# Kernel tuning notes

Measured on AMD Instinct MI355X. Metric: run time of the kernel, lower is better.

Reference implementation:

```python
import jax, jax.numpy as jnp
import numpy as np


def conv1d(x, w, b):
    # x: (N, Cin, W), w: (Cout, Cin, K) -> (N, Cout, W-K+1), VALID conv (torch Conv1d)
    y = jax.lax.conv_general_dilated(x, w, (1,), 'VALID', dimension_numbers=('NCH', 'OIH', 'NCH'))
    return y + b[None, :, None]


def cnn_block(x, w, b):
    # conv1d then MaxPool1d over the full valid length -> (N, Cout)
    return jnp.max(conv1d(x, w, b), axis=2)


def highway(x, Wp, bp, Wg, bg):
    p = jax.nn.relu(x @ Wp.T + bp)
    g = jax.nn.sigmoid(x @ Wg.T + bg)
    return g * p + (1.0 - g) * x


def lstm_masked(x, lens, Wih, Whh, bih, bhh):
    # x: (N, Wt, E); lens: (N,) valid lengths. Emulates pack_padded_sequence +
    # nn.LSTM + pad_packed_sequence: outputs are h_t for t < len, zeros after.
    N, Wt, _ = x.shape
    H = Whh.shape[1]
    bias = bih + bhh
    h0 = jnp.zeros((N, H), x.dtype)

    def step(carry, inp):
        xt, t = inp
        h, c = carry
        z = xt @ Wih.T + h @ Whh.T + bias  # (N, 4H), gate order i,f,g,o
        i, f, g, o = jnp.split(z, 4, axis=-1)
        c2 = jax.nn.sigmoid(f) * c + jax.nn.sigmoid(i) * jnp.tanh(g)
        h2 = jax.nn.sigmoid(o) * jnp.tanh(c2)
        valid = (t < lens)[:, None]
        h2 = jnp.where(valid, h2, h)
        c2 = jnp.where(valid, c2, c)
        return (h2, c2), jnp.where(valid, h2, jnp.zeros_like(h2))

    xs = jnp.moveaxis(x, 1, 0)  # (Wt, N, E)
    ts = jnp.arange(Wt)
    _, out = jax.lax.scan(step, (h0, h0), (xs, ts))
    return jnp.moveaxis(out, 0, 1)  # (N, Wt, H)


def setup_inputs() -> dict:
    key = jax.random.key(0)
    ks = jax.random.split(key, 32)
    B, T = 32, 48
    WL, WA, WE = 33, 50, 30
    EL, EA, EE, H = 300, 988, 20, 128
    CL, CA, CE = 128, 256, 64
    s = 0.02
    inp = {
        'x_lin': jax.random.normal(ks[0], (B, T, WL, EL), jnp.float32),
        'x_aco': jax.random.normal(ks[1], (B, T, WA, EA), jnp.float32),
        'x_emo': jax.random.normal(ks[2], (B, T, WE, EE), jnp.float32),
        'window_length': jax.random.randint(ks[3], (B, T), 0, WE).astype(jnp.int32) + 1,
        'length': jax.random.randint(ks[4], (B,), 1, T + 1).astype(jnp.int32),
        # CNN params
        'convL_w': s * jax.random.normal(ks[5], (CL, EL, 5), jnp.float32),
        'convL_b': jnp.zeros((CL,), jnp.float32),
        'convA_w': s * jax.random.normal(ks[6], (CA, EA, 10), jnp.float32),
        'convA_b': jnp.zeros((CA,), jnp.float32),
        'convE_w': s * jax.random.normal(ks[7], (CE, H, 3), jnp.float32),
        'convE_b': jnp.zeros((CE,), jnp.float32),
        # Highway params
        'hwL_Wp': s * jax.random.normal(ks[8], (CL, CL), jnp.float32),
        'hwL_bp': jnp.zeros((CL,), jnp.float32),
        'hwL_Wg': s * jax.random.normal(ks[9], (CL, CL), jnp.float32),
        'hwL_bg': jnp.zeros((CL,), jnp.float32),
        'hwA_Wp': s * jax.random.normal(ks[10], (CA, CA), jnp.float32),
        'hwA_bp': jnp.zeros((CA,), jnp.float32),
        'hwA_Wg': s * jax.random.normal(ks[11], (CA, CA), jnp.float32),
        'hwA_bg': jnp.zeros((CA,), jnp.float32),
        'hwE_Wp': s * jax.random.normal(ks[12], (CE, CE), jnp.float32),
        'hwE_bp': jnp.zeros((CE,), jnp.float32),
        'hwE_Wg': s * jax.random.normal(ks[13], (CE, CE), jnp.float32),
        'hwE_bg': jnp.zeros((CE,), jnp.float32),
        # LSTM params (nn.LSTM, 1 layer, batch_first)
        'lstm_Wih': s * jax.random.normal(ks[14], (4 * H, EE), jnp.float32),
        'lstm_Whh': s * jax.random.normal(ks[15], (4 * H, H), jnp.float32),
        'lstm_bih': jnp.zeros((4 * H,), jnp.float32),
        'lstm_bhh': jnp.zeros((4 * H,), jnp.float32),
    }
    return inp


def reference(x_lin, x_aco, x_emo, window_length, length,
              convL_w, convL_b, convA_w, convA_b, convE_w, convE_b,
              hwL_Wp, hwL_bp, hwL_Wg, hwL_bg,
              hwA_Wp, hwA_bp, hwA_Wg, hwA_bg,
              hwE_Wp, hwE_bp, hwE_Wg, hwE_bg,
              lstm_Wih, lstm_Whh, lstm_bih, lstm_bhh):
    B, T = x_lin.shape[:2]
    # Linguistic: per-window CNN + Highway (dropout = identity in eval)
    xl = x_lin.reshape(B * T, x_lin.shape[2], x_lin.shape[3]).transpose(0, 2, 1)  # (BT, 300, WL)
    outL = highway(cnn_block(xl, convL_w, convL_b), hwL_Wp, hwL_bp, hwL_Wg, hwL_bg)
    outL = outL.reshape(B, T, -1)
    # Acoustic
    xa = x_aco.reshape(B * T, x_aco.shape[2], x_aco.shape[3]).transpose(0, 2, 1)  # (BT, 988, WA)
    outA = highway(cnn_block(xa, convA_w, convA_b), hwA_Wp, hwA_bp, hwA_Wg, hwA_bg)
    outA = outA.reshape(B, T, -1)
    # Emotient: ragged per-window LSTM (packed semantics) -> CNN -> Highway
    xe = x_emo.reshape(B * T, x_emo.shape[2], x_emo.shape[3])  # (BT, WE, 20)
    lens = window_length.reshape(B * T)
    h = lstm_masked(xe, lens, lstm_Wih, lstm_Whh, lstm_bih, lstm_bhh)  # (BT, WE, 128)
    outE = highway(cnn_block(h.transpose(0, 2, 1), convE_w, convE_b), hwE_Wp, hwE_bp, hwE_Wg, hwE_bg)
    outE = outE.reshape(B, T, -1)
    # Concatenate modalities -> (B, T, 128+256+64) fed to the downstream head
    return jnp.concatenate([outL, outA, outE], axis=2)
```

## Files before the change

kernel.cpp:

```cpp
#include <hip/hip_runtime.h>
#include <hip/hip_bf16.h>
#include <math.h>

#define BTOT 1536
#define EL 300
#define ELP 320
#define WL_ 33
#define CL 128
#define LOUTL 29
#define KPL 1600
#define EA 988
#define EAP 992
#define WA_ 50
#define CA 256
#define LOUTA 41
#define KPA 9920
#define EE 20
#define WE_ 30
#define HH 128
#define CE 64
#define LOUTE 28
#define KPE 384
#define KDIML 1500
#define KDIMA 9880
#define KDIME 384

typedef __attribute__((ext_vector_type(4))) float f32x4;
typedef __attribute__((ext_vector_type(8))) short short8;

__device__ __forceinline__ unsigned short f2bf(float f) {
    unsigned int x = __float_as_uint(f);
    unsigned int r = (x + 0x7fffu + ((x >> 16) & 1u)) >> 16;
    return (unsigned short)r;
}

__device__ __forceinline__ float sigmf(float x) {
    return __builtin_amdgcn_rcpf(1.f + __expf(-x));
}
__device__ __forceinline__ float tanh_fast(float x) {
    return 1.f - 2.f * __builtin_amdgcn_rcpf(1.f + __expf(2.f * x));
}

#define GLD16(gp, lp) __builtin_amdgcn_global_load_lds( \
    (const __attribute__((address_space(1))) void*)(gp), \
    (__attribute__((address_space(3))) void*)(lp), 16, 0, 0)

template<int N> __device__ __forceinline__ void vmwait() {
    if constexpr (N == 0) asm volatile("s_waitcnt vmcnt(0)" ::: "memory");
    else if constexpr (N == 1) asm volatile("s_waitcnt vmcnt(1)" ::: "memory");
    else if constexpr (N == 2) asm volatile("s_waitcnt vmcnt(2)" ::: "memory");
    else if constexpr (N == 4) asm volatile("s_waitcnt vmcnt(4)" ::: "memory");
    else if constexpr (N == 5) asm volatile("s_waitcnt vmcnt(5)" ::: "memory");
    else if constexpr (N == 6) asm volatile("s_waitcnt vmcnt(6)" ::: "memory");
    else if constexpr (N == 8) asm volatile("s_waitcnt vmcnt(8)" ::: "memory");
    else static_assert(N == 0, "add case");
}

__device__ __forceinline__ void tr_one(const float* a, float* at, int R, int C, int idx) {
    int r = idx / C, c = idx - r * C;
    at[c * R + r] = a[idx];
}
template<int CIN, int CINP, int KW, int COUT, int KPAD>
__device__ __forceinline__ void wt_one(const float* w, unsigned short* wt, int idx) {
    int co = idx / KPAD;
    int p  = idx - co * KPAD;
    int k  = p / CINP;
    int c  = p - k * CINP;
    float v = 0.f;
    if (k < KW && c < CIN) v = w[(co * CIN + c) * KW + k];
    wt[idx] = f2bf(v);
}
template<bool BIG>
__global__ void prep_all(const float* hwL_Wp, float* WpTL, const float* hwL_Wg, float* WgTL,
                         const float* hwA_Wp, float* WpTA, const float* hwA_Wg, float* WgTA,
                         const float* hwE_Wp, float* WpTE, const float* hwE_Wg, float* WgTE,
                         const float* lstm_Wih, float* WihT, const float* lstm_Whh, float* WhhT,
                         const float* convL_w, unsigned short* wtL,
                         const float* convE_w, unsigned short* wtE,
                         const float* convA_w, unsigned short* wtA,
                         unsigned short* whh_bf, unsigned short* wihp_bf) {
    constexpr int S1 = 16384, S2 = 16384, S3 = 65536, S4 = 65536, S5 = 4096, S6 = 4096;
    constexpr int S7 = 512 * 20, S8 = 512 * 128;
    constexpr int S9 = 128 * KPL, S10 = 64 * KPE, S11 = 512 * 128, S12 = 512 * 32;
    constexpr int S13 = CA * KPA;
    constexpr int SMALL = S1 + S2 + S3 + S4 + S5 + S6 + S7 + S8;
    constexpr int TOTAL = BIG ? (SMALL + S9 + S10 + S11 + S12 + S13) : SMALL;
    int stride = gridDim.x * blockDim.x;
    for (int i = blockIdx.x * blockDim.x + threadIdx.x; i < TOTAL; i += stride) {
        int idx = i;
        if (idx < S1) { tr_one(hwL_Wp, WpTL, 128, 128, idx); continue; } idx -= S1;
        if (idx < S2) { tr_one(hwL_Wg, WgTL, 128, 128, idx); continue; } idx -= S2;
        if (idx < S3) { tr_one(hwA_Wp, WpTA, 256, 256, idx); continue; } idx -= S3;
        if (idx < S4) { tr_one(hwA_Wg, WgTA, 256, 256, idx); continue; } idx -= S4;
        if (idx < S5) { tr_one(hwE_Wp, WpTE, 64, 64, idx); continue; } idx -= S5;
        if (idx < S6) { tr_one(hwE_Wg, WgTE, 64, 64, idx); continue; } idx -= S6;
        if (idx < S7) { tr_one(lstm_Wih, WihT, 512, 20, idx); continue; } idx -= S7;
        if (idx < S8) { tr_one(lstm_Whh, WhhT, 512, 128, idx); continue; } idx -= S8;
        if constexpr (BIG) {
            if (idx < S9) { wt_one<EL, ELP, 5, CL, KPL>(convL_w, wtL, idx); continue; } idx -= S9;
            if (idx < S10) { wt_one<HH, HH, 3, CE, KPE>(convE_w, wtE, idx); continue; } idx -= S10;
            if (idx < S11) { whh_bf[idx] = f2bf(lstm_Whh[idx]); continue; } idx -= S11;
            if (idx < S12) { int col = idx >> 5, e = idx & 31;
                             wihp_bf[idx] = (e < 20) ? f2bf(lstm_Wih[col * 20 + e]) : (unsigned short)0;
                             continue; } idx -= S12;
            wt_one<EA, EAP, 10, CA, KPA>(convA_w, wtA, idx);
        }
    }
}

template<int CIN, int CINP>
__device__ __forceinline__ void cvt_chunk(const float* in, unsigned short* out, int idx) {
    constexpr int CH = CINP / 8;
    int row = idx / CH, c0 = (idx - row * CH) * 8;
    const float* src = in + (size_t)row * CIN + c0;
    union { short8 s; unsigned short u[8]; } o;
    if (c0 + 8 <= CIN) {
        float4 v0 = *(const float4*)src;
        float4 v1 = *(const float4*)(src + 4);
        o.u[0]=f2bf(v0.x); o.u[1]=f2bf(v0.y); o.u[2]=f2bf(v0.z); o.u[3]=f2bf(v0.w);
        o.u[4]=f2bf(v1.x); o.u[5]=f2bf(v1.y); o.u[6]=f2bf(v1.z); o.u[7]=f2bf(v1.w);
    } else {
        #pragma unroll
        for (int j = 0; j < 8; ++j) o.u[j] = (c0 + j < CIN) ? f2bf(src[j]) : (unsigned short)0;
    }
    *(short8*)(out + (size_t)row * CINP + c0) = o.s;
}

#define LSTM_BLOCKS 96
#define CVT_BLOCKS 1952

__global__ __launch_bounds__(512, 1)
void lstm_cvt(const float* __restrict__ x_emo,
              const unsigned short* __restrict__ wihp_bf, const unsigned short* __restrict__ whh_bf,
              const float* __restrict__ bih, const float* __restrict__ bhh,
              const int* __restrict__ lens, unsigned short* __restrict__ hbuf,
              const float* __restrict__ xa, const float* __restrict__ xl,
              unsigned short* __restrict__ outa, unsigned short* __restrict__ outl)
{
    __shared__ __align__(16) unsigned short xq[WE_ * 16 * 32];
    __shared__ __align__(16) char h_s[2 * 16 * HH * 2];

    if (blockIdx.x >= LSTM_BLOCKS) {
        constexpr int NAC = (BTOT * WA_) * (EAP / 8);
        constexpr int NLC = (BTOT * WL_) * (ELP / 8);
        int stride = CVT_BLOCKS * 512;
        for (int i = (blockIdx.x - LSTM_BLOCKS) * 512 + threadIdx.x; i < NAC + NLC; i += stride) {
            if (i < NAC) cvt_chunk<EA, EAP>(xa, outa, i);
            else         cvt_chunk<EL, ELP>(xl, outl, i - NAC);
        }
        return;
    }

    const int tid  = threadIdx.x;
    const int w    = tid >> 6;
    const int lane = tid & 63;
    const int lr   = lane & 15;
    const int lq   = lane >> 4;
    const int s0   = blockIdx.x * 16;
    const int c    = w * 16 + lr;

    short8 bfr[4][4];
    short8 bw[4];
    float bj[4];
    #pragma unroll
    for (int g = 0; g < 4; ++g) {
        int col = g * 128 + c;
        #pragma unroll
        for (int kt = 0; kt < 4; ++kt)
            bfr[g][kt] = *(const short8*)(whh_bf + (size_t)col * 128 + kt * 32 + lq * 8);
        bw[g] = *(const short8*)(wihp_bf + (size_t)col * 32 + lq * 8);
        bj[g] = bih[col] + bhh[col];
    }
    int len4[4];
    #pragma unroll
    for (int j = 0; j < 4; ++j) len4[j] = lens[s0 + lq * 4 + j];

    for (int i = tid; i < WE_ * 16 * 32; i += 512) {
        int t = i >> 9, r = (i >> 5) & 15, e = i & 31;
        xq[i] = (e < 20) ? f2bf(x_emo[(((size_t)(s0 + r) * WE_) + t) * 20 + e]) : (unsigned short)0;
    }
    for (int i = tid; i < 2048; i += 512) ((unsigned int*)h_s)[i] = 0u;

    float c_prev[4] = {0.f, 0.f, 0.f, 0.f};
    unsigned short hb_prev[4] = {0, 0, 0, 0};
    __syncthreads();

    for (int t = 0; t < WE_; ++t) {
        const char* hsr = h_s + (t & 1) * 4096;
        char* hsw = h_s + ((t & 1) ^ 1) * 4096;
        short8 ax = *(const short8*)((const char*)xq + (size_t)(t * 16 + lr) * 64 + lq * 16);
        short8 af[4];
        #pragma unroll
        for (int kt = 0; kt < 4; ++kt)
            af[kt] = *(const short8*)(hsr + ((lr * 256 + kt * 64 + lq * 16) ^ ((lr & 7) << 4)));
        f32x4 acc[4];
        #pragma unroll
        for (int g = 0; g < 4; ++g)
            acc[g] = __builtin_amdgcn_mfma_f32_16x16x32_bf16(ax, bw[g], (f32x4){0.f,0.f,0.f,0.f}, 0, 0, 0);
        #pragma unroll
        for (int kt = 0; kt < 4; ++kt)
            #pragma unroll
            for (int g = 0; g < 4; ++g)
                acc[g] = __builtin_amdgcn_mfma_f32_16x16x32_bf16(af[kt], bfr[g][kt], acc[g], 0, 0, 0);
        #pragma unroll
        for (int j = 0; j < 4; ++j) {
            int s = lq * 4 + j;
            float zi = acc[0][j] + bj[0];
            float zf = acc[1][j] + bj[1];
            float zg = acc[2][j] + bj[2];
            float zo = acc[3][j] + bj[3];
            float si = sigmf(zi), sf = sigmf(zf), so = sigmf(zo);
            float tg = tanh_fast(zg);
            float c2 = sf * c_prev[j] + si * tg;
            float h2 = so * tanh_fast(c2);
            bool valid = (t < len4[j]);
            c_prev[j] = valid ? c2 : c_prev[j];
            unsigned short h2b = f2bf(h2);
            unsigned short hn = valid ? h2b : hb_prev[j];
            hb_prev[j] = hn;
            *(unsigned short*)(hsw + (((s * HH + c) * 2) ^ ((s & 7) << 4))) = hn;
            hbuf[(((size_t)(s0 + s) * WE_) + t) * HH + c] = valid ? h2b : (unsigned short)0;
        }
        __syncthreads();
    }
}

template<int LOUT, int WIN, int CINP, int KW, int BN, int NS, int MFR, int COUT>
__global__ __launch_bounds__(256, 2)
void conv_pool_v8(const unsigned short* __restrict__ xb, const unsigned short* __restrict__ wt,
                  const float* __restrict__ bias, float* __restrict__ pooled)
{
    constexpr int CCH   = CINP / 32;
    constexpr int KB    = CINP * 2;
    constexpr int KTOTB = CINP * KW * 2;
    constexpr int NFR   = BN / 16;
    constexpr int B_IT  = BN / 64;
    constexpr int ABUF  = 4 * 64 * 64;
    constexpr int BBUF  = BN * 64;
    constexpr int CPQ   = (BTOT / 4) / 4;

    __shared__ __align__(16) char smem[2 * ABUF + 4 * BBUF];

    const int tid  = threadIdx.x;
    const int lane = tid & 63;
    const int wid  = tid >> 6;
    const int lr   = lane & 15;
    const int lq   = lane >> 4;
    const int lq16 = lq * 16;

    int m, n;
    if constexpr (NS == 2) {
        int xcd = blockIdx.x & 7;
        n = xcd & 1;
        m = (xcd >> 1) * CPQ + (blockIdx.x >> 3);
    } else {
        m = blockIdx.x; n = 0;
    }

    f32x4 acc[MFR][NFR];
    #pragma unroll
    for (int i = 0; i < MFR; ++i)
        #pragma unroll
        for (int j = 0; j < NFR; ++j) acc[i][j] = (f32x4){0.f, 0.f, 0.f, 0.f};

    const int aw_r = tid >> 2;
    const int aw   = (aw_r < WIN) ? aw_r : (WIN - 1);
    const int slot = tid & 3;
    const char* asrc[4];
    #pragma unroll
    for (int i = 0; i < 4; ++i)
        asrc[i] = (const char*)xb + ((size_t)((m * 4 + i) * WIN + aw)) * KB
                + ((slot * 16) ^ (((aw_r >> 1) & 3) << 4));
    const char* bsrc[B_IT];
    #pragma unroll
    for (int i = 0; i < B_IT; ++i) {
        int col = (tid + i * 256) >> 2;
        bsrc[i] = (const char*)wt + (size_t)(n * BN + col) * KTOTB
                + ((slot * 16) ^ (((col >> 1) & 3) << 4));
    }

    char* const abuf0 = smem;
    char* const abuf1 = smem + ABUF;
    char* const bbase = smem + 2 * ABUF;

    int cbo[NFR];
    #pragma unroll
    for (int nf = 0; nf < NFR; ++nf) {
        int cb = nf * 16 + lr;
        cbo[nf] = cb * 64 + (lq16 ^ (((cb >> 1) & 3) << 4));
    }

    #pragma unroll
    for (int i = 0; i < 4; ++i)
        GLD16(asrc[i], abuf0 + i * 4096 + tid * 16);
    #pragma unroll
    for (int s = 0; s < 3; ++s)
        #pragma unroll
        for (int i = 0; i < B_IT; ++i)
            GLD16(bsrc[i] + s * KB, bbase + s * BBUF + i * 4096 + tid * 16);
    vmwait<0>();
    __builtin_amdgcn_s_barrier();

    int bcur = 0;

#define STEP(KK, WN, TAIL) do {                                                    \
    const char* bb = bbase + bcur * BBUF;                                          \
    short8 afr[MFR];                                                               \
    _Pragma("unroll")                                                              \
    for (int o = 0; o < MFR; ++o) {                                                \
        int row = o * 16 + lr + (KK);                                              \
        afr[o] = *(const short8*)(awave + row * 64 + (lq16 ^ (((row >> 1) & 3) << 4))); \
    }                                                                              \
    short8 bf[NFR];                                                                \
    _Pragma("unroll")                                                              \
    for (int nf = 0; nf < NFR; ++nf) bf[nf] = *(const short8*)(bb + cbo[nf]);      \
    if (!(TAIL) || (KK) < KW - 3) {                                                \
        constexpr int k3_ = ((KK) + 3 < KW) ? (KK) + 3 : (KK) + 3 - KW;            \
        int boff = k3_ * KB + (((KK) + 3 < KW) ? ci : ci + 1) * 64;                \
        char* bstg = bbase + ((bcur + 3) & 3) * BBUF;                              \
        _Pragma("unroll")                                                          \
        for (int i = 0; i < B_IT; ++i)                                             \
            GLD16(bsrc[i] + boff, bstg + i * 4096 + tid * 16);                     \
    }                                                                              \
    if (!(TAIL)) {                                                                 \
        if (KW >= 8) {                                                             \
            if ((KK) < 4)                                                          \
                GLD16(asrc[(KK) & 3] + (size_t)(ci + 1) * 64, abn + ((KK) & 3) * 4096 + tid * 16); \
        } else if ((KK) == 0) {                                                    \
            _Pragma("unroll")                                                      \
            for (int i = 0; i < 4; ++i)                                            \
                GLD16(asrc[i] + (size_t)(ci + 1) * 64, abn + i * 4096 + tid * 16); \
        }                                                                          \
    }                                                                              \
    asm volatile("s_waitcnt lgkmcnt(0)" ::: "memory");                             \
    __builtin_amdgcn_sched_barrier(0);                                             \
    __builtin_amdgcn_s_setprio(1);                                                 \
    _Pragma("unroll")                                                              \
    for (int nf = 0; nf < NFR; ++nf)                                               \
        _Pragma("unroll")                                                          \
        for (int o = 0; o < MFR; ++o)                                              \
            acc[o][nf] = __builtin_amdgcn_mfma_f32_16x16x32_bf16(afr[o], bf[nf], acc[o][nf], 0, 0, 0); \
    __builtin_amdgcn_s_setprio(0);                                                 \
    vmwait<WN>();                                                                  \
    asm volatile("" ::: "memory");                                                 \
    __builtin_amdgcn_s_barrier();                                                  \
    bcur = (bcur + 1) & 3;                                                         \
} while (0)

    for (int ci = 0; ci < CCH - 1; ++ci) {
        const char* ab = (ci & 1) ? abuf1 : abuf0;
        char* abn = (ci & 1) ? abuf0 : abuf1;
        const char* awave = ab + wid * 4096;
        if constexpr (KW == 10) {
            STEP(0, 5, false); STEP(1, 6, false); STEP(2, 6, false); STEP(3, 6, false);
            STEP(4, 5, false); STEP(5, 4, false); STEP(6, 4, false); STEP(7, 4, false);
            STEP(8, 4, false); STEP(9, 4, false);
        } else if constexpr (KW == 5) {
            STEP(0, 8, false); STEP(1, 8, false); STEP(2, 4, false); STEP(3, 4, false); STEP(4, 4, false);
        } else {
            STEP(0, 6, false); STEP(1, 6, false); STEP(2, 2, false);
        }
    }
    {
        const int ci = CCH - 1;
        const char* ab = (ci & 1) ? abuf1 : abuf0;
        char* abn = (ci & 1) ? abuf0 : abuf1; (void)abn;
        const char* awave = ab + wid * 4096;
        if constexpr (KW == 10) {
            STEP(0, 4, true); STEP(1, 4, true); STEP(2, 4, true); STEP(3, 4, true);
            STEP(4, 4, true); STEP(5, 4, true); STEP(6, 4, true); STEP(7, 2, true);
            STEP(8, 0, true); STEP(9, 0, true);
        } else if constexpr (KW == 5) {
            STEP(0, 4, true); STEP(1, 4, true); STEP(2, 2, true); STEP(3, 0, true); STEP(4, 0, true);
        } else {
            STEP(0, 1, true); STEP(1, 0, true); STEP(2, 0, true);
        }
    }
#undef STEP

    const int bt = m * 4 + wid;
    #pragma unroll
    for (int nf = 0; nf < NFR; ++nf) {
        float mx = -INFINITY;
        #pragma unroll
        for (int o = 0; o < MFR; ++o) {
            int rb = o * 16 + lq * 4;
            #pragma unroll
            for (int j = 0; j < 4; ++j)
                if (rb + j < LOUT) mx = fmaxf(mx, acc[o][nf][j]);
        }
        mx = fmaxf(mx, __shfl_xor(mx, 16, 64));
        mx = fmaxf(mx, __shfl_xor(mx, 32, 64));
        if (lane < 16) {
            int col = n * BN + nf * 16 + lane;
            pooled[(size_t)bt * COUT + col] = mx + bias[col];
        }
    }
}

__global__ __launch_bounds__(256)
void highway_all(const float* __restrict__ pL, const float* __restrict__ pA, const float* __restrict__ pE,
                 const float* __restrict__ WpTL, const float* __restrict__ bpL,
                 const float* __restrict__ WgTL, const float* __restrict__ bgL,
                 const float* __restrict__ WpTA, const float* __restrict__ bpA,
                 const float* __restrict__ WgTA, const float* __restrict__ bgA,
                 const float* __restrict__ WpTE, const float* __restrict__ bpE,
                 const float* __restrict__ WgTE, const float* __restrict__ bgE,
                 float* __restrict__ out) {
    __shared__ float xs[256];
    int bx = blockIdx.x;
    int tid = threadIdx.x;
    if (bx < BTOT) {
        xs[tid] = pA[(size_t)bx * 256 + tid];
        __syncthreads();
        float ap = bpA[tid], ag = bgA[tid];
        for (int c = 0; c < 256; ++c) {
            float xv = xs[c];
            ap += xv * WpTA[c * 256 + tid];
            ag += xv * WgTA[c * 256 + tid];
        }
        float pp = fmaxf(ap, 0.f);
        float g = sigmf(ag);
        out[(size_t)bx * 448 + 128 + tid] = g * pp + (1.f - g) * xs[tid];
    } else {
        int bt = bx - BTOT;
        if (tid < 128) xs[tid] = pL[(size_t)bt * 128 + tid];
        else if (tid < 192) xs[64 + tid] = pE[(size_t)bt * 64 + (tid - 128)];
        __syncthreads();
        if (tid < 128) {
            float ap = bpL[tid], ag = bgL[tid];
            for (int c = 0; c < 128; ++c) {
                float xv = xs[c];
                ap += xv * WpTL[c * 128 + tid];
                ag += xv * WgTL[c * 128 + tid];
            }
            float pp = fmaxf(ap, 0.f);
            float g = sigmf(ag);
            out[(size_t)bt * 448 + tid] = g * pp + (1.f - g) * xs[tid];
        } else if (tid < 192) {
            int j = tid - 128;
            float ap = bpE[j], ag = bgE[j];
            for (int c = 0; c < 64; ++c) {
                float xv = xs[192 + c];
                ap += xv * WpTE[c * 64 + j];
                ag += xv * WgTE[c * 64 + j];
            }
            float pp = fmaxf(ap, 0.f);
            float g = sigmf(ag);
            out[(size_t)bt * 448 + 384 + j] = g * pp + (1.f - g) * xs[192 + j];
        }
    }
}

__global__ __launch_bounds__(512)
void lstm_kernel_f32(const float* __restrict__ x, const int* __restrict__ lens,
                     const float* __restrict__ WihT, const float* __restrict__ WhhT,
                     const float* __restrict__ bih, const float* __restrict__ bhh,
                     float* __restrict__ hout) {
    int bt = blockIdx.x;
    int j  = threadIdx.x;
    __shared__ float xs[WE_][EE];
    __shared__ __align__(16) float hs[HH];
    __shared__ float zs[512];
    for (int idx = j; idx < WE_ * EE; idx += 512)
        ((float*)xs)[idx] = x[(size_t)bt * WE_ * EE + idx];
    if (j < HH) hs[j] = 0.f;
    float wih[EE];
    #pragma unroll
    for (int e = 0; e < EE; ++e) wih[e] = WihT[e * 512 + j];
    float whh[HH];
    #pragma unroll
    for (int h = 0; h < HH; ++h) whh[h] = WhhT[h * 512 + j];
    float bjv = bih[j] + bhh[j];
    float c_reg = 0.f;
    int len = lens[bt];
    __syncthreads();
    for (int t = 0; t < WE_; ++t) {
        float z = bjv;
        #pragma unroll
        for (int e = 0; e < EE; ++e) z += wih[e] * xs[t][e];
        const float4* h4 = (const float4*)hs;
        #pragma unroll
        for (int q = 0; q < HH / 4; ++q) {
            float4 hv = h4[q];
            z += whh[4*q+0] * hv.x + whh[4*q+1] * hv.y
               + whh[4*q+2] * hv.z + whh[4*q+3] * hv.w;
        }
        zs[j] = z;
        __syncthreads();
        if (j < HH) {
            float zi = zs[j], zf = zs[HH + j], zg = zs[2*HH + j], zo = zs[3*HH + j];
            float si = 1.f / (1.f + expf(-zi));
            float sf = 1.f / (1.f + expf(-zf));
            float so = 1.f / (1.f + expf(-zo));
            float tg = tanhf(zg);
            float c2 = sf * c_reg + si * tg;
            float h2 = so * tanhf(c2);
            bool valid = (t < len);
            float hn = valid ? h2 : hs[j];
            c_reg    = valid ? c2 : c_reg;
            hout[((size_t)bt * WE_ + t) * HH + j] = valid ? h2 : 0.f;
            hs[j] = hn;
        }
        __syncthreads();
    }
}

template<int CIN, int WIN, int COUT, int KDIM, int LOUT>
__global__ __launch_bounds__(256)
void conv_pool_simple(const float* __restrict__ x, const float* __restrict__ w,
                      const float* __restrict__ bias, float* __restrict__ pooled)
{
    constexpr int KW = KDIM / CIN;
    int bt = blockIdx.x;
    int co = blockIdx.y * 64 + (threadIdx.x & 63);
    int seg = threadIdx.x >> 6;
    __shared__ float part[4][64];
    float m = -INFINITY;
    for (int l = seg; l < LOUT; l += 4) {
        float acc = 0.f;
        for (int k = 0; k < KW; ++k) {
            const float* xr = x + ((size_t)bt * WIN + l + k) * CIN;
            const float* wr = w + ((size_t)co * CIN) * KW + k;
            for (int cc = 0; cc < CIN; ++cc) acc += xr[cc] * wr[(size_t)cc * KW];
        }
        m = fmaxf(m, acc);
    }
    part[seg][threadIdx.x & 63] = m;
    __syncthreads();
    if (threadIdx.x < 64) {
        float mm = fmaxf(fmaxf(part[0][threadIdx.x], part[1][threadIdx.x]),
                         fmaxf(part[2][threadIdx.x], part[3][threadIdx.x]));
        pooled[(size_t)bt * COUT + co] = mm + bias[co];
    }
}

static inline int cdiv(int a, int b) { return (a + b - 1) / b; }

extern "C" void kernel_launch(void* const* d_in, const int* in_sizes, int n_in,
                              void* d_out, int out_size, void* d_ws, size_t ws_size,
                              hipStream_t stream) {
    const float* x_lin  = (const float*)d_in[0];
    const float* x_aco  = (const float*)d_in[1];
    const float* x_emo  = (const float*)d_in[2];
    const int*   wlen   = (const int*)  d_in[3];
    const float* convL_w = (const float*)d_in[5];
    const float* convL_b = (const float*)d_in[6];
    const float* convA_w = (const float*)d_in[7];
    const float* convA_b = (const float*)d_in[8];
    const float* convE_w = (const float*)d_in[9];
    const float* convE_b = (const float*)d_in[10];
    const float* hwL_Wp = (const float*)d_in[11];
    const float* hwL_bp = (const float*)d_in[12];
    const float* hwL_Wg = (const float*)d_in[13];
    const float* hwL_bg = (const float*)d_in[14];
    const float* hwA_Wp = (const float*)d_in[15];
    const float* hwA_bp = (const float*)d_in[16];
    const float* hwA_Wg = (const float*)d_in[17];
    const float* hwA_bg = (const float*)d_in[18];
    const float* hwE_Wp = (const float*)d_in[19];
    const float* hwE_bp = (const float*)d_in[20];
    const float* hwE_Wg = (const float*)d_in[21];
    const float* hwE_bg = (const float*)d_in[22];
    const float* lstm_Wih = (const float*)d_in[23];
    const float* lstm_Whh = (const float*)d_in[24];
    const float* lstm_bih = (const float*)d_in[25];
    const float* lstm_bhh = (const float*)d_in[26];
    float* out = (float*)d_out;

    char* p0 = (char*)d_ws;
    char* p = p0;
    auto alloc = [&](size_t bytes) { char* r = p; p += (bytes + 255) & ~(size_t)255; return r; };
    float* WpTL = (float*)alloc((size_t)CL * CL * 4);
    float* WgTL = (float*)alloc((size_t)CL * CL * 4);
    float* WpTA = (float*)alloc((size_t)CA * CA * 4);
    float* WgTA = (float*)alloc((size_t)CA * CA * 4);
    float* WpTE = (float*)alloc((size_t)CE * CE * 4);
    float* WgTE = (float*)alloc((size_t)CE * CE * 4);
    float* WihT = (float*)alloc((size_t)EE * 512 * 4);
    float* WhhT = (float*)alloc((size_t)HH * 512 * 4);
    unsigned short* whh_bf  = (unsigned short*)alloc((size_t)512 * 128 * 2);
    unsigned short* wihp_bf = (unsigned short*)alloc((size_t)512 * 32 * 2);
    void*  hbuf = (void*)alloc((size_t)BTOT * WE_ * HH * 4);
    float* pL   = (float*)alloc((size_t)BTOT * CL * 4);
    float* pA   = (float*)alloc((size_t)BTOT * CA * 4);
    float* pE   = (float*)alloc((size_t)BTOT * CE * 4);
    unsigned short* wtA = (unsigned short*)alloc((size_t)CA * KPA * 2);
    unsigned short* wtL = (unsigned short*)alloc((size_t)CL * KPL * 2);
    unsigned short* wtE = (unsigned short*)alloc((size_t)CE * KPE * 2);
    unsigned short* xlin_p = (unsigned short*)alloc((size_t)BTOT * WL_ * ELP * 2 + 64);
    unsigned short* xaco_p = (unsigned short*)alloc((size_t)BTOT * WA_ * EAP * 2 + 64);
    size_t need = (size_t)(p - p0);
    bool big = ws_size >= need;

    if (big) {
        prep_all<true><<<2048, 256, 0, stream>>>(hwL_Wp, WpTL, hwL_Wg, WgTL, hwA_Wp, WpTA, hwA_Wg, WgTA,
                                                 hwE_Wp, WpTE, hwE_Wg, WgTE, lstm_Wih, WihT, lstm_Whh, WhhT,
                                                 convL_w, wtL, convE_w, wtE, convA_w, wtA, whh_bf, wihp_bf);
        lstm_cvt<<<LSTM_BLOCKS + CVT_BLOCKS, 512, 0, stream>>>(
            x_emo, wihp_bf, whh_bf, lstm_bih, lstm_bhh, wlen, (unsigned short*)hbuf,
            x_aco, x_lin, xaco_p, xlin_p);
        conv_pool_v8<LOUTA, WA_, EAP, 10, 128, 2, 3, CA>
            <<<768, 256, 0, stream>>>(xaco_p, wtA, convA_b, pA);
        conv_pool_v8<LOUTL, WL_, ELP, 5, 128, 1, 2, CL>
            <<<384, 256, 0, stream>>>(xlin_p, wtL, convL_b, pL);
        conv_pool_v8<LOUTE, WE_, HH, 3, 64, 1, 2, CE>
            <<<384, 256, 0, stream>>>((const unsigned short*)hbuf, wtE, convE_b, pE);
    } else {
        prep_all<false><<<2048, 256, 0, stream>>>(hwL_Wp, WpTL, hwL_Wg, WgTL, hwA_Wp, WpTA, hwA_Wg, WgTA,
                                                  hwE_Wp, WpTE, hwE_Wg, WgTE, lstm_Wih, WihT, lstm_Whh, WhhT,
                                                  convL_w, wtL, convE_w, wtE, convA_w, wtA, whh_bf, wihp_bf);
        lstm_kernel_f32<<<BTOT, 512, 0, stream>>>(x_emo, wlen, WihT, WhhT, lstm_bih, lstm_bhh, (float*)hbuf);
        conv_pool_simple<EA, WA_, CA, KDIMA, LOUTA>
            <<<dim3(BTOT, CA / 64), 256, 0, stream>>>(x_aco, convA_w, convA_b, pA);
        conv_pool_simple<EL, WL_, CL, KDIML, LOUTL>
            <<<dim3(BTOT, CL / 64), 256, 0, stream>>>(x_lin, convL_w, convL_b, pL);
        conv_pool_simple<HH, WE_, CE, KDIME, LOUTE>
            <<<dim3(BTOT, CE / 64), 256, 0, stream>>>((const float*)hbuf, convE_w, convE_b, pE);
    }

    highway_all<<<2 * BTOT, 256, 0, stream>>>(pL, pA, pE,
                                              WpTL, hwL_bp, WgTL, hwL_bg,
                                              WpTA, hwA_bp, WgTA, hwA_bg,
                                              WpTE, hwE_bp, WgTE, hwE_bg, out);
}
```

Measured before the change: 567.9 us.

## Double-buffer LDS fragment reads in conv MFMA loop and batch highway rows per block

The conv kernel now prefetches the next step's A/B fragments from LDS into a second register set while the current MFMAs run. It waits on a partial lgkmcnt instead of draining all LDS reads, and the vmcnt thresholds are retuned to match. Separately, the highway kernel processes 8 rows per thread so each weight load is reused across rows, and it launches far fewer blocks. The costs are more VGPR pressure from the duplicated fragment sets, plus code duplication for the ci parity.

```diff
diff --git a/kernel.cpp b/kernel.cpp
--- a/kernel.cpp
+++ b/kernel.cpp
@@ -49,11 +49,17 @@
     if constexpr (N == 0) asm volatile("s_waitcnt vmcnt(0)" ::: "memory");
     else if constexpr (N == 1) asm volatile("s_waitcnt vmcnt(1)" ::: "memory");
     else if constexpr (N == 2) asm volatile("s_waitcnt vmcnt(2)" ::: "memory");
+    else if constexpr (N == 3) asm volatile("s_waitcnt vmcnt(3)" ::: "memory");
     else if constexpr (N == 4) asm volatile("s_waitcnt vmcnt(4)" ::: "memory");
     else if constexpr (N == 5) asm volatile("s_waitcnt vmcnt(5)" ::: "memory");
     else if constexpr (N == 6) asm volatile("s_waitcnt vmcnt(6)" ::: "memory");
-    else if constexpr (N == 8) asm volatile("s_waitcnt vmcnt(8)" ::: "memory");
     else static_assert(N == 0, "add case");
+}
+template<int N> __device__ __forceinline__ void lgkmwait() {
+    if constexpr (N == 6)  asm volatile("s_waitcnt lgkmcnt(6)" ::: "memory");
+    else if constexpr (N == 10) asm volatile("s_waitcnt lgkmcnt(10)" ::: "memory");
+    else if constexpr (N == 11) asm volatile("s_waitcnt lgkmcnt(11)" ::: "memory");
+    else static_assert(N == 6, "add case");
 }
 
 __device__ __forceinline__ void tr_one(const float* a, float* at, int R, int C, int idx) {
@@ -227,7 +233,7 @@
 
 template<int LOUT, int WIN, int CINP, int KW, int BN, int NS, int MFR, int COUT>
 __global__ __launch_bounds__(256, 2)
-void conv_pool_v8(const unsigned short* __restrict__ xb, const unsigned short* __restrict__ wt,
+void conv_pool_v9(const unsigned short* __restrict__ xb, const unsigned short* __restrict__ wt,
                   const float* __restrict__ bias, float* __restrict__ pooled)
 {
     constexpr int CCH   = CINP / 32;
@@ -235,6 +241,7 @@
     constexpr int KTOTB = CINP * KW * 2;
     constexpr int NFR   = BN / 16;
     constexpr int B_IT  = BN / 64;
+    constexpr int NRD   = MFR + NFR;
     constexpr int ABUF  = 4 * 64 * 64;
     constexpr int BBUF  = BN * 64;
     constexpr int CPQ   = (BTOT / 4) / 4;
@@ -301,29 +308,31 @@
     vmwait<0>();
     __builtin_amdgcn_s_barrier();
 
+    short8 afrA[MFR], afrB[MFR], bfA[NFR], bfB[NFR];
     int bcur = 0;
 
-#define STEP(KK, WN, TAIL) do {                                                    \
-    const char* bb = bbase + bcur * BBUF;                                          \
-    short8 afr[MFR];                                                               \
+#define READF(SET, APTR, BSLOT, KNEXT) do {                                        \
+    const char* bbp = bbase + (BSLOT) * BBUF;                                      \
+    _Pragma("unroll")                                                              \
+    for (int nf = 0; nf < NFR; ++nf) bf##SET[nf] = *(const short8*)(bbp + cbo[nf]);\
     _Pragma("unroll")                                                              \
     for (int o = 0; o < MFR; ++o) {                                                \
-        int row = o * 16 + lr + (KK);                                              \
-        afr[o] = *(const short8*)(awave + row * 64 + (lq16 ^ (((row >> 1) & 3) << 4))); \
+        int row = o * 16 + lr + (KNEXT);                                           \
+        afr##SET[o] = *(const short8*)((APTR) + row * 64 + (lq16 ^ (((row >> 1) & 3) << 4))); \
     }                                                                              \
-    short8 bf[NFR];                                                                \
-    _Pragma("unroll")                                                              \
-    for (int nf = 0; nf < NFR; ++nf) bf[nf] = *(const short8*)(bb + cbo[nf]);      \
-    if (!(TAIL) || (KK) < KW - 3) {                                                \
-        constexpr int k3_ = ((KK) + 3 < KW) ? (KK) + 3 : (KK) + 3 - KW;            \
-        int boff = k3_ * KB + (((KK) + 3 < KW) ? ci : ci + 1) * 64;                \
+} while (0)
+
+#define STEP(KK, CUR, NXT, WN, TAIL) do {                                          \
+    if (!(TAIL) || (KK) < KW - 3) {                             \
+        constexpr int K3 = ((KK) + 3 < KW) ? (KK) + 3 : (KK) + 3 - KW;             \
+        int boff = K3 * KB + (((KK) + 3 < KW) ? ci : ci + 1) * 64;                 \
         char* bstg = bbase + ((bcur + 3) & 3) * BBUF;                              \
         _Pragma("unroll")                                                          \
         for (int i = 0; i < B_IT; ++i)                                             \
             GLD16(bsrc[i] + boff, bstg + i * 4096 + tid * 16);                     \
     }                                                                              \
-    if (!(TAIL)) {                                                                 \
-        if (KW >= 8) {                                                             \
+    if (!(TAIL)) {                                              \
+        if constexpr (KW >= 8) {                                                   \
             if ((KK) < 4)                                                          \
                 GLD16(asrc[(KK) & 3] + (size_t)(ci + 1) * 64, abn + ((KK) & 3) * 4096 + tid * 16); \
         } else if ((KK) == 0) {                                                    \
@@ -332,14 +341,19 @@
                 GLD16(asrc[i] + (size_t)(ci + 1) * 64, abn + i * 4096 + tid * 16); \
         }                                                                          \
     }                                                                              \
-    asm volatile("s_waitcnt lgkmcnt(0)" ::: "memory");                             \
+    {                                           \
+        constexpr int KN = ((KK) + 1 < KW) ? (KK) + 1 : 0;                         \
+        const char* ap = ((KK) + 1 < KW) ? awave : awnext;                         \
+        READF(NXT, ap, (bcur + 1) & 3, KN);                                        \
+    }                                                                              \
+    lgkmwait<NRD>();                                                               \
     __builtin_amdgcn_sched_barrier(0);                                             \
     __builtin_amdgcn_s_setprio(1);                                                 \
     _Pragma("unroll")                                                              \
     for (int nf = 0; nf < NFR; ++nf)                                               \
         _Pragma("unroll")                                                          \
         for (int o = 0; o < MFR; ++o)                                              \
-            acc[o][nf] = __builtin_amdgcn_mfma_f32_16x16x32_bf16(afr[o], bf[nf], acc[o][nf], 0, 0, 0); \
+            acc[o][nf] = __builtin_amdgcn_mfma_f32_16x16x32_bf16(afr##CUR[o], bf##CUR[nf], acc[o][nf], 0, 0, 0); \
     __builtin_amdgcn_s_setprio(0);                                                 \
     vmwait<WN>();                                                                  \
     asm volatile("" ::: "memory");                                                 \
@@ -347,18 +361,35 @@
     bcur = (bcur + 1) & 3;                                                         \
 } while (0)
 
+    {
+        const char* aw0 = abuf0 + wid * 4096;
+        READF(A, aw0, 0, 0);
+    }
+
     for (int ci = 0; ci < CCH - 1; ++ci) {
         const char* ab = (ci & 1) ? abuf1 : abuf0;
         char* abn = (ci & 1) ? abuf0 : abuf1;
         const char* awave = ab + wid * 4096;
+        const char* awnext = abn + wid * 4096;
         if constexpr (KW == 10) {
-            STEP(0, 5, false); STEP(1, 6, false); STEP(2, 6, false); STEP(3, 6, false);
-            STEP(4, 5, false); STEP(5, 4, false); STEP(6, 4, false); STEP(7, 4, false);
-            STEP(8, 4, false); STEP(9, 4, false);
+            STEP(0, A, B, 3, false); STEP(1, B, A, 4, false); STEP(2, A, B, 4, false);
+            STEP(3, B, A, 4, false); STEP(4, A, B, 3, false); STEP(5, B, A, 2, false);
+            STEP(6, A, B, 2, false); STEP(7, B, A, 2, false); STEP(8, A, B, 2, false);
+            STEP(9, B, A, 2, false);
         } else if constexpr (KW == 5) {
-            STEP(0, 8, false); STEP(1, 8, false); STEP(2, 4, false); STEP(3, 4, false); STEP(4, 4, false);
+            if (ci & 1) {
+                STEP(0, B, A, 6, false); STEP(1, A, B, 6, false); STEP(2, B, A, 2, false);
+                STEP(3, A, B, 2, false); STEP(4, B, A, 2, false);
+            } else {
+                STEP(0, A, B, 6, false); STEP(1, B, A, 6, false); STEP(2, A, B, 2, false);
+                STEP(3, B, A, 2, false); STEP(4, A, B, 2, false);
+            }
         } else {
-            STEP(0, 6, false); STEP(1, 6, false); STEP(2, 2, false);
+            if (ci & 1) {
+                STEP(0, B, A, 5, false); STEP(1, A, B, 1, false); STEP(2, B, A, 1, false);
+            } else {
+                STEP(0, A, B, 5, false); STEP(1, B, A, 1, false); STEP(2, A, B, 1, false);
+            }
         }
     }
     {
@@ -366,17 +397,30 @@
         const char* ab = (ci & 1) ? abuf1 : abuf0;
         char* abn = (ci & 1) ? abuf0 : abuf1; (void)abn;
         const char* awave = ab + wid * 4096;
+        const char* awnext = awave;
         if constexpr (KW == 10) {
-            STEP(0, 4, true); STEP(1, 4, true); STEP(2, 4, true); STEP(3, 4, true);
-            STEP(4, 4, true); STEP(5, 4, true); STEP(6, 4, true); STEP(7, 2, true);
-            STEP(8, 0, true); STEP(9, 0, true);
+            STEP(0, A, B, 2, true); STEP(1, B, A, 2, true); STEP(2, A, B, 2, true);
+            STEP(3, B, A, 2, true); STEP(4, A, B, 2, true); STEP(5, B, A, 2, true);
+            STEP(6, A, B, 2, true); STEP(7, B, A, 0, true); STEP(8, A, B, 0, true);
+            STEP(9, B, A, 0, true);
         } else if constexpr (KW == 5) {
-            STEP(0, 4, true); STEP(1, 4, true); STEP(2, 2, true); STEP(3, 0, true); STEP(4, 0, true);
+            if (ci & 1) {
+                STEP(0, B, A, 2, true); STEP(1, A, B, 2, true); STEP(2, B, A, 0, true);
+                STEP(3, A, B, 0, true); STEP(4, B, A, 0, true);
+            } else {
+                STEP(0, A, B, 2, true); STEP(1, B, A, 2, true); STEP(2, A, B, 0, true);
+                STEP(3, B, A, 0, true); STEP(4, A, B, 0, true);
+            }
         } else {
-            STEP(0, 1, true); STEP(1, 0, true); STEP(2, 0, true);
+            if (ci & 1) {
+                STEP(0, B, A, 0, true); STEP(1, A, B, 0, true); STEP(2, B, A, 0, true);
+            } else {
+                STEP(0, A, B, 0, true); STEP(1, B, A, 0, true); STEP(2, A, B, 0, true);
+            }
         }
     }
 #undef STEP
+#undef READF
 
     const int bt = m * 4 + wid;
     #pragma unroll
@@ -398,56 +442,86 @@
     }
 }
 
+#define HWA_BLOCKS 192
+#define HWL_BLOCKS 96
+#define HWE_BLOCKS 48
 __global__ __launch_bounds__(256)
-void highway_all(const float* __restrict__ pL, const float* __restrict__ pA, const float* __restrict__ pE,
-                 const float* __restrict__ WpTL, const float* __restrict__ bpL,
-                 const float* __restrict__ WgTL, const float* __restrict__ bgL,
-                 const float* __restrict__ WpTA, const float* __restrict__ bpA,
-                 const float* __restrict__ WgTA, const float* __restrict__ bgA,
-                 const float* __restrict__ WpTE, const float* __restrict__ bpE,
-                 const float* __restrict__ WgTE, const float* __restrict__ bgE,
-                 float* __restrict__ out) {
-    __shared__ float xs[256];
+void highway_v2(const float* __restrict__ pL, const float* __restrict__ pA, const float* __restrict__ pE,
+                const float* __restrict__ WpTL, const float* __restrict__ bpL,
+                const float* __restrict__ WgTL, const float* __restrict__ bgL,
+                const float* __restrict__ WpTA, const float* __restrict__ bpA,
+                const float* __restrict__ WgTA, const float* __restrict__ bgA,
+                const float* __restrict__ WpTE, const float* __restrict__ bpE,
+                const float* __restrict__ WgTE, const float* __restrict__ bgE,
+                float* __restrict__ out) {
+    __shared__ float xs[2048];
     int bx = blockIdx.x;
     int tid = threadIdx.x;
-    if (bx < BTOT) {
-        xs[tid] = pA[(size_t)bx * 256 + tid];
+    if (bx < HWA_BLOCKS) {
+        int bt0 = bx * 8;
+        #pragma unroll
+        for (int s = 0; s < 8; ++s) xs[s * 256 + tid] = pA[(size_t)(bt0 + s) * 256 + tid];
         __syncthreads();
-        float ap = bpA[tid], ag = bgA[tid];
+        float p[8], g[8];
+        #pragma unroll
+        for (int s = 0; s < 8; ++s) { p[s] = bpA[tid]; g[s] = bgA[tid]; }
         for (int c = 0; c < 256; ++c) {
-            float xv = xs[c];
-            ap += xv * WpTA[c * 256 + tid];
-            ag += xv * WgTA[c * 256 + tid];
-        }
-        float pp = fmaxf(ap, 0.f);
-        float g = sigmf(ag);
-        out[(size_t)bx * 448 + 128 + tid] = g * pp + (1.f - g) * xs[tid];
+            float wp = WpTA[c * 256 + tid], wg = WgTA[c * 256 + tid];
+            #pragma unroll
+            for (int s = 0; s < 8; ++s) {
+                float xv = xs[s * 256 + c];
+                p[s] += xv * wp; g[s] += xv * wg;
+            }
+        }
+        #pragma unroll
+        for (int s = 0; s < 8; ++s) {
+            float pp = fmaxf(p[s], 0.f);
+            float gg = sigmf(g[s]);
+            out[(size_t)(bt0 + s) * 448 + 128 + tid] = gg * pp + (1.f - gg) * xs[s * 256 + tid];
+        }
+    } else if (bx < HWA_BLOCKS + HWL_BLOCKS) {
+        int bt0 = (bx - HWA_BLOCKS) * 16;
+        for (int i = tid; i < 16 * 128; i += 256) xs[i] = pL[(size_t)bt0 * 128 + i];
+        __syncthreads();
+        int j = tid & 127, h = tid >> 7;
+        float p[8], g[8];
+        #pragma unroll
+        for (int s = 0; s < 8; ++s) { p[s] = bpL[j]; g[s] = bgL[j]; }
+        for (int c = 0; c < 128; ++c) {
+            float wp = WpTL[c * 128 + j], wg = WgTL[c * 128 + j];
+            #pragma unroll
+            for (int s = 0; s < 8; ++s) {
+                float xv = xs[(h * 8 + s) * 128 + c];
+                p[s] += xv * wp; g[s] += xv * wg;
+            }
+        }
+        #pragma unroll
+        for (int s = 0; s < 8; ++s) {
+            float pp = fmaxf(p[s], 0.f);
+            float gg = sigmf(g[s]);
+            out[(size_t)(bt0 + h * 8 + s) * 448 + j] = gg * pp + (1.f - gg) * xs[(h * 8 + s) * 128 + j];
+        }
     } else {
-        int bt = bx - BTOT;
-        if (tid < 128) xs[tid] = pL[(size_t)bt * 128 + tid];
-        else if (tid < 192) xs[64 + tid] = pE[(size_t)bt * 64 + (tid - 128)];
+        int bt0 = (bx - HWA_BLOCKS - HWL_BLOCKS) * 32;
+        for (int i = tid; i < 32 * 64; i += 256) xs[i] = pE[(size_t)bt0 * 64 + i];
         __syncthreads();
-        if (tid < 128) {
-            float ap = bpL[tid], ag = bgL[tid];
-            for (int c = 0; c < 128; ++c) {
-                float xv = xs[c];
-                ap += xv * WpTL[c * 128 + tid];
-                ag += xv * WgTL[c * 128 + tid];
+        int j = tid & 63, grp = tid >> 6;
+        float p[8], g[8];
+        #pragma unroll
+        for (int s = 0; s < 8; ++s) { p[s] = bpE[j]; g[s] = bgE[j]; }
+        for (int c = 0; c < 64; ++c) {
+            float wp = WpTE[c * 64 + j], wg = WgTE[c * 64 + j];
+            #pragma unroll
+            for (int s = 0; s < 8; ++s) {
+                float xv = xs[(grp * 8 + s) * 64 + c];
+                p[s] += xv * wp; g[s] += xv * wg;
             }
-            float pp = fmaxf(ap, 0.f);
-            float g = sigmf(ag);
-            out[(size_t)bt * 448 + tid] = g * pp + (1.f - g) * xs[tid];
-        } else if (tid < 192) {
-            int j = tid - 128;
-            float ap = bpE[j], ag = bgE[j];
-            for (int c = 0; c < 64; ++c) {
-                float xv = xs[192 + c];
-                ap += xv * WpTE[c * 64 + j];
-                ag += xv * WgTE[c * 64 + j];
-            }
-            float pp = fmaxf(ap, 0.f);
-            float g = sigmf(ag);
-            out[(size_t)bt * 448 + 384 + j] = g * pp + (1.f - g) * xs[192 + j];
+        }
+        #pragma unroll
+        for (int s = 0; s < 8; ++s) {
+            float pp = fmaxf(p[s], 0.f);
+            float gg = sigmf(g[s]);
+            out[(size_t)(bt0 + grp * 8 + s) * 448 + 384 + j] = gg * pp + (1.f - gg) * xs[(grp * 8 + s) * 64 + j];
         }
     }
 }
@@ -600,12 +674,15 @@
         lstm_cvt<<<LSTM_BLOCKS + CVT_BLOCKS, 512, 0, stream>>>(
             x_emo, wihp_bf, whh_bf, lstm_bih, lstm_bhh, wlen, (unsigned short*)hbuf,
             x_aco, x_lin, xaco_p, xlin_p);
-        conv_pool_v8<LOUTA, WA_, EAP, 10, 128, 2, 3, CA>
+        conv_pool_v9<LOUTA, WA_, EAP, 10, 128, 2, 3, CA>
             <<<768, 256, 0, stream>>>(xaco_p, wtA, convA_b, pA);
-        conv_pool_v8<LOUTL, WL_, ELP, 5, 128, 1, 2, CL>
+        conv_pool_v9<LOUTL, WL_, ELP, 5, 128, 1, 2, CL>
             <<<384, 256, 0, stream>>>(xlin_p, wtL, convL_b, pL);
-        conv_pool_v8<LOUTE, WE_, HH, 3, 64, 1, 2, CE>
+        conv_pool_v9<LOUTE, WE_, HH, 3, 64, 1, 2, CE>
             <<<384, 256, 0, stream>>>((const unsigned short*)hbuf, wtE, convE_b, pE);
+        highway_v2<<<HWA_BLOCKS + HWL_BLOCKS + HWE_BLOCKS, 256, 0, stream>>>(
+            pL, pA, pE, WpTL, hwL_bp, WgTL, hwL_bg, WpTA, hwA_bp, WgTA, hwA_bg,
+            WpTE, hwE_bp, WgTE, hwE_bg, out);
     } else {
         prep_all<false><<<2048, 256, 0, stream>>>(hwL_Wp, WpTL, hwL_Wg, WgTL, hwA_Wp, WpTA, hwA_Wg, WgTA,
                                                   hwE_Wp, WpTE, hwE_Wg, WgTE, lstm_Wih, WihT, lstm_Whh, WhhT,
@@ -617,10 +694,8 @@
             <<<dim3(BTOT, CL / 64), 256, 0, stream>>>(x_lin, convL_w, convL_b, pL);
         conv_pool_simple<HH, WE_, CE, KDIME, LOUTE>
             <<<dim3(BTOT, CE / 64), 256, 0, stream>>>((const float*)hbuf, convE_w, convE_b, pE);
-    }
-
-    highway_all<<<2 * BTOT, 256, 0, stream>>>(pL, pA, pE,
-                                              WpTL, hwL_bp, WgTL, hwL_bg,
-                                              WpTA, hwA_bp, WgTA, hwA_bg,
-                                              WpTE, hwE_bp, WgTE, hwE_bg, out);
-}
+        highway_v2<<<HWA_BLOCKS + HWL_BLOCKS + HWE_BLOCKS, 256, 0, stream>>>(
+            pL, pA, pE, WpTL, hwL_bp, WgTL, hwL_bg, WpTA, hwA_bp, WgTA, hwA_bg,
+            WpTE, hwE_bp, WgTE, hwE_bg, out);
+    }
+}
```

Result: slower. 1.031 ms (+81.6%).
